# Performance work log

Hardware: AMD Instinct MI355X
Metric: run time of the kernel (lower is better)

The kernel has to match this reference:

```python
import jax, jax.numpy as jnp
import numpy as np

L, H, D, FF, T, S, N = 4, 16, 1024, 4096, 256, 256, 16
NEG = -1e9

def layer_norm(x, g, b):
    mu = jnp.mean(x, axis=-1, keepdims=True)
    var = jnp.var(x, axis=-1, keepdims=True)
    return (x - mu) / jnp.sqrt(var + 1e-5) * g + b

def mha(q_in, k_in, v_in, wq, bq, wk, bk, wv, bv, wo, bo, mask):
    # q_in: [T,N,D]; k_in/v_in: [S,N,D]
    t, n, d = q_in.shape
    s = k_in.shape[0]
    hd = d // H
    scale = hd ** -0.5
    q = (q_in @ wq.T + bq) * scale
    k = k_in @ wk.T + bk
    v = v_in @ wv.T + bv
    q = q.reshape(t, n, H, hd)
    k = k.reshape(s, n, H, hd)
    v = v.reshape(s, n, H, hd)
    scores = jnp.einsum('tnhd,snhd->nhts', q, k)  # [N,H,T,S]
    if mask is not None:
        scores = scores + mask  # mask [T,S] broadcasts
    a = jax.nn.softmax(scores, axis=-1)
    o = jnp.einsum('nhts,snhd->tnhd', a, v).reshape(t, n, d)
    return o @ wo.T + bo

def forward(tgt, memory, sa_wq, sa_bq, sa_wk, sa_bk, sa_wv, sa_bv, sa_wo, sa_bo,
            ca_wq, ca_bq, ca_wk, ca_bk, ca_wv, ca_bv, ca_wo, ca_bo,
            w1, b1, w2, b2, ln1_g, ln1_b, ln2_g, ln2_b, ln3_g, ln3_b, lnf_g, lnf_b):
    t = tgt.shape[0]
    causal = jnp.where(jnp.triu(jnp.ones((t, t), bool), 1), jnp.float32(NEG), jnp.float32(0.0))
    x = tgt
    for i in range(L):
        sa = mha(x, x, x, sa_wq[i], sa_bq[i], sa_wk[i], sa_bk[i], sa_wv[i], sa_bv[i], sa_wo[i], sa_bo[i], causal)
        x = layer_norm(x + sa, ln1_g[i], ln1_b[i])
        ca = mha(x, memory, memory, ca_wq[i], ca_bq[i], ca_wk[i], ca_bk[i], ca_wv[i], ca_bv[i], ca_wo[i], ca_bo[i], None)
        x = layer_norm(x + ca, ln2_g[i], ln2_b[i])
        ff = jax.nn.relu(x @ w1[i].T + b1[i]) @ w2[i].T + b2[i]
        x = layer_norm(x + ff, ln3_g[i], ln3_b[i])
    return layer_norm(x, lnf_g, lnf_b)

def setup_inputs() -> dict:
    key = jax.random.key(0)
    ks = iter(jax.random.split(key, 40))
    def nrm(shape, s):
        return (jax.random.normal(next(ks), shape, jnp.float32) * s).astype(jnp.float32)
    sd = D ** -0.5
    inp = {
        'tgt': nrm((T, N, D), 1.0),
        'memory': nrm((S, N, D), 1.0),
    }
    for pre in ('sa', 'ca'):
        for nm in ('wq', 'wk', 'wv', 'wo'):
            inp[f'{pre}_{nm}'] = nrm((L, D, D), sd)
        for nm in ('bq', 'bk', 'bv', 'bo'):
            inp[f'{pre}_{nm}'] = jnp.zeros((L, D), jnp.float32)
    inp['w1'] = nrm((L, FF, D), sd)
    inp['b1'] = jnp.zeros((L, FF), jnp.float32)
    inp['w2'] = nrm((L, D, FF), FF ** -0.5)
    inp['b2'] = jnp.zeros((L, D), jnp.float32)
    for nm in ('ln1', 'ln2', 'ln3'):
        inp[f'{nm}_g'] = jnp.ones((L, D), jnp.float32)
        inp[f'{nm}_b'] = jnp.zeros((L, D), jnp.float32)
    inp['lnf_g'] = jnp.ones((D,), jnp.float32)
    inp['lnf_b'] = jnp.zeros((D,), jnp.float32)
    return inp

def reference(tgt, memory, sa_wq, sa_bq, sa_wk, sa_bk, sa_wv, sa_bv, sa_wo, sa_bo,
              ca_wq, ca_bq, ca_wk, ca_bk, ca_wv, ca_bv, ca_wo, ca_bo,
              w1, b1, w2, b2, ln1_g, ln1_b, ln2_g, ln2_b, ln3_g, ln3_b, lnf_g, lnf_b):
    return forward(tgt, memory, sa_wq, sa_bq, sa_wk, sa_bk, sa_wv, sa_bv, sa_wo, sa_bo,
                   ca_wq, ca_bq, ca_wk, ca_bk, ca_wv, ca_bv, ca_wo, ca_bo,
                   w1, b1, w2, b2, ln1_g, ln1_b, ln2_g, ln2_b, ln3_g, ln3_b, lnf_g, lnf_b)
```

## Files before the change

kernel.cpp:

```cpp
#include <hip/hip_runtime.h>


typedef __attribute__((ext_vector_type(4))) float f32x4;
typedef __attribute__((ext_vector_type(8))) short bf16x8;
typedef __attribute__((ext_vector_type(4))) unsigned short u16x4;
typedef __attribute__((ext_vector_type(4))) unsigned int   u32x4;

__device__ __forceinline__ unsigned short f2bf(float f) {
    unsigned int u = __builtin_bit_cast(unsigned int, f);
    u += 0x7fffu + ((u >> 16) & 1u);
    return (unsigned short)(u >> 16);
}

__device__ __forceinline__ void gll16(const unsigned short* g, unsigned short* l) {
    auto* gp = reinterpret_cast<const __attribute__((address_space(1))) unsigned int*>(
        reinterpret_cast<uintptr_t>(g));
    auto* lp = reinterpret_cast<__attribute__((address_space(3))) unsigned int*>(
        reinterpret_cast<uintptr_t>(l));
    __builtin_amdgcn_global_load_lds(gp, lp, 16, 0, 0);
}

__device__ __forceinline__ void gemm_body(
    const unsigned short* __restrict__ A,
    const unsigned short* __restrict__ Bw,
    const float* __restrict__ bias,
    unsigned short* __restrict__ outb,
    float* __restrict__ po,
    int N, int lda, int klen, int mode,
    int m0, int n0, int kz,
    unsigned short (*Al)[128 * 32], unsigned short (*Bl)[128 * 32])
{
    const int tid  = threadIdx.x;
    const int lane = tid & 63;
    const int w    = tid >> 6;
    const int wr   = (w >> 1) * 64;
    const int wc   = (w & 1) * 64;
    const int l15  = lane & 15;
    const int l4   = lane >> 4;

    const int srow = w * 16 + (lane >> 2);
    const int scol = ((lane & 3) ^ ((srow >> 1) & 3)) * 8;
    const unsigned short* ag = A  + (size_t)(m0 + srow) * lda + kz + scol;
    const unsigned short* bg = Bw + (size_t)(n0 + srow) * lda + kz + scol;
    const size_t jstep = (size_t)64 * lda;
    const int lbase = (w * 16) * 32;

    int aoff[4], boff[4];
    #pragma unroll
    for (int i = 0; i < 4; ++i) {
        const int ra = wr + i * 16 + l15;
        const int rb = wc + i * 16 + l15;
        aoff[i] = ra * 32 + ((l4 ^ ((ra >> 1) & 3)) * 8);
        boff[i] = rb * 32 + ((l4 ^ ((rb >> 1) & 3)) * 8);
    }

    f32x4 acc[4][4];
    #pragma unroll
    for (int mi = 0; mi < 4; ++mi)
        #pragma unroll
        for (int ni = 0; ni < 4; ++ni)
            acc[mi][ni] = (f32x4){0.f, 0.f, 0.f, 0.f};

    #pragma unroll
    for (int j = 0; j < 2; ++j) {
        gll16(ag + j * jstep, &Al[0][lbase + j * 64 * 32]);
        gll16(bg + j * jstep, &Bl[0][lbase + j * 64 * 32]);
    }
    __syncthreads();

    const int nt = klen >> 5;
    int cur = 0;
    for (int t = 0; t < nt; ++t) {
        if (t + 1 < nt) {
            ag += 32; bg += 32;
            #pragma unroll
            for (int j = 0; j < 2; ++j) {
                gll16(ag + j * jstep, &Al[cur ^ 1][lbase + j * 64 * 32]);
                gll16(bg + j * jstep, &Bl[cur ^ 1][lbase + j * 64 * 32]);
            }
        }
        const unsigned short* ac = &Al[cur][0];
        const unsigned short* bc = &Bl[cur][0];
        bf16x8 af[4], bf[4];
        #pragma unroll
        for (int i = 0; i < 4; ++i) af[i] = *reinterpret_cast<const bf16x8*>(&ac[aoff[i]]);
        #pragma unroll
        for (int i = 0; i < 4; ++i) bf[i] = *reinterpret_cast<const bf16x8*>(&bc[boff[i]]);
        #pragma unroll
        for (int mi = 0; mi < 4; ++mi)
            #pragma unroll
            for (int ni = 0; ni < 4; ++ni)
                acc[mi][ni] = __builtin_amdgcn_mfma_f32_16x16x32_bf16(af[mi], bf[ni], acc[mi][ni], 0, 0, 0);
        __syncthreads();
        cur ^= 1;
    }

    #pragma unroll
    for (int mi = 0; mi < 4; ++mi) {
        #pragma unroll
        for (int ni = 0; ni < 4; ++ni) {
            const int col = n0 + wc + ni * 16 + l15;
            const float bs = (mode == 3) ? 0.f : bias[col];
            #pragma unroll
            for (int r = 0; r < 4; ++r) {
                const int row = m0 + wr + mi * 16 + l4 * 4 + r;
                const float val = acc[mi][ni][r] + bs;
                if (mode == 0)      outb[(size_t)row * N + col] = f2bf(val);
                else if (mode == 1) outb[(size_t)row * N + col] = f2bf(fmaxf(val, 0.f));
                else                po[(size_t)row * N + col] = val;
            }
        }
    }
}

__global__ __launch_bounds__(256, 4) void gemm128(
    const unsigned short* __restrict__ A,
    const unsigned short* __restrict__ Bw,
    const float* __restrict__ bias,
    unsigned short* __restrict__ outb,
    float* __restrict__ outf0,
    float* __restrict__ outf1,
    int N, int lda, int klen, int mode)
{
    __shared__ unsigned short Al[2][128 * 32];
    __shared__ unsigned short Bl[2][128 * 32];
    const int gx   = gridDim.x;
    const int orig = blockIdx.y * gx + blockIdx.x;
    const int xcd  = orig & 7;
    const int lin  = orig >> 3;
    const int m0   = (xcd * 4 + (lin & 3)) * 128;
    const int n0   = (lin >> 2) * 128;
    const int kz   = blockIdx.z * klen;
    float* po = (blockIdx.z == 0) ? outf0 : outf1;
    gemm_body(A, Bw, bias, outb, po, N, lda, klen, mode, m0, n0, kz, Al, Bl);
}

__global__ __launch_bounds__(256, 4) void gemm128_ca(
    const unsigned short* __restrict__ A0, const unsigned short* __restrict__ A1,
    const unsigned short* __restrict__ B0, const unsigned short* __restrict__ B1,
    const float* __restrict__ bias0, const float* __restrict__ bias1,
    unsigned short* __restrict__ out0, unsigned short* __restrict__ out1,
    int lda, int klen)
{
    __shared__ unsigned short Al[2][128 * 32];
    __shared__ unsigned short Bl[2][128 * 32];
    const int grp = (blockIdx.x >= 8);
    const int bx  = blockIdx.x - (grp ? 8 : 0);
    const int lgx = grp ? 16 : 8;
    const int orig = blockIdx.y * lgx + bx;
    const int xcd  = orig & 7;
    const int lin  = orig >> 3;
    const int m0   = (xcd * 4 + (lin & 3)) * 128;
    const int n0   = (lin >> 2) * 128;
    gemm_body(grp ? A1 : A0, grp ? B1 : B0, grp ? bias1 : bias0,
              grp ? out1 : out0, nullptr, grp ? 2048 : 1024, lda, klen, 0,
              m0, n0, 0, Al, Bl);
}

__global__ __launch_bounds__(128) void attn_fused(
    const unsigned short* __restrict__ Q, int qs,
    const unsigned short* __restrict__ Kb, int ks_,
    const unsigned short* __restrict__ Vb, int vs,
    unsigned short* __restrict__ O,
    int causal)
{
    __shared__ unsigned short Kl[8][256][8];
    __shared__ unsigned short Vt[32][64][8];
    __shared__ unsigned short Pl[2][32][16][8];
    const int tid   = threadIdx.x;
    const int lane  = tid & 63;
    const int w     = tid >> 6;
    const int bxi   = blockIdx.x;
    const int n     = bxi >> 5;
    const int h     = (bxi >> 1) & 15;
    const int thalf = bxi & 1;
    const int l15   = lane & 15;
    const int l4    = lane >> 4;
    const size_t hoff = (size_t)h * 64;

    #pragma unroll
    for (int i = 0; i < 16; ++i) {
        const int e = i * 128 + tid;
        const int s = e >> 3;
        const int c = e & 7;
        u32x4 kv = *reinterpret_cast<const u32x4*>(&Kb[((size_t)s * 16 + n) * ks_ + hoff + c * 8]);
        *reinterpret_cast<u32x4*>(&Kl[c][s][0]) = kv;
        u32x4 vv = *reinterpret_cast<const u32x4*>(&Vb[((size_t)s * 16 + n) * vs + hoff + c * 8]);
        const unsigned short* ve = reinterpret_cast<const unsigned short*>(&vv);
        #pragma unroll
        for (int j = 0; j < 8; ++j)
            Vt[s >> 3][c * 8 + j][s & 7] = ve[j];
    }
    __syncthreads();

    for (int ch = 0; ch < 4; ++ch) {
        const int t0 = thalf * 128 + w * 64 + ch * 16;
        bf16x8 qa[2];
        #pragma unroll
        for (int ks = 0; ks < 2; ++ks)
            qa[ks] = *reinterpret_cast<const bf16x8*>(
                &Q[((size_t)(t0 + l15) * 16 + n) * qs + hoff + ks * 32 + l4 * 8]);

        f32x4 sc[16];
        #pragma unroll
        for (int st = 0; st < 16; ++st) {
            if (causal && st * 16 > t0 + 15) {
                sc[st] = (f32x4){-1e9f, -1e9f, -1e9f, -1e9f};
                continue;
            }
            f32x4 a = (f32x4){0.f, 0.f, 0.f, 0.f};
            #pragma unroll
            for (int ks = 0; ks < 2; ++ks) {
                bf16x8 kf = *reinterpret_cast<const bf16x8*>(&Kl[ks * 4 + l4][st * 16 + l15][0]);
                a = __builtin_amdgcn_mfma_f32_16x16x32_bf16(qa[ks], kf, a, 0, 0, 0);
            }
            sc[st] = a;
        }
        if (causal) {
            #pragma unroll
            for (int st = 0; st < 16; ++st) {
                const int sg = st * 16 + l15;
                #pragma unroll
                for (int r = 0; r < 4; ++r) {
                    const int tg = t0 + l4 * 4 + r;
                    if (sg > tg) sc[st][r] = -1e9f;
                }
            }
        }
        #pragma unroll
        for (int r = 0; r < 4; ++r) {
            float mx = -3.0e38f;
            #pragma unroll
            for (int st = 0; st < 16; ++st) mx = fmaxf(mx, sc[st][r]);
            #pragma unroll
            for (int dd = 1; dd < 16; dd <<= 1) mx = fmaxf(mx, __shfl_xor(mx, dd, 64));
            float sum = 0.f;
            #pragma unroll
            for (int st = 0; st < 16; ++st) {
                const float e = __expf(sc[st][r] - mx);
                sc[st][r] = e;
                sum += e;
            }
            #pragma unroll
            for (int dd = 1; dd < 16; dd <<= 1) sum += __shfl_xor(sum, dd, 64);
            const float inv = 1.f / sum;
            const int rl = l4 * 4 + r;
            #pragma unroll
            for (int st = 0; st < 16; ++st) {
                const int sg = st * 16 + l15;
                Pl[w][sg >> 3][rl][sg & 7] = f2bf(sc[st][r] * inv);
            }
        }
        f32x4 oacc[4];
        #pragma unroll
        for (int dt = 0; dt < 4; ++dt) oacc[dt] = (f32x4){0.f, 0.f, 0.f, 0.f};
        #pragma unroll
        for (int kt = 0; kt < 8; ++kt) {
            if (causal && kt * 32 > t0 + 15) continue;
            bf16x8 pa = *reinterpret_cast<const bf16x8*>(&Pl[w][kt * 4 + l4][l15][0]);
            #pragma unroll
            for (int dt = 0; dt < 4; ++dt) {
                bf16x8 vf = *reinterpret_cast<const bf16x8*>(&Vt[kt * 4 + l4][dt * 16 + l15][0]);
                oacc[dt] = __builtin_amdgcn_mfma_f32_16x16x32_bf16(pa, vf, oacc[dt], 0, 0, 0);
            }
        }
        #pragma unroll
        for (int dt = 0; dt < 4; ++dt)
            #pragma unroll
            for (int r = 0; r < 4; ++r)
                O[((size_t)(t0 + l4 * 4 + r) * 16 + n) * 1024 + hoff + dt * 16 + l15] = f2bf(oacc[dt][r]);
    }
}

__device__ __forceinline__ void ln_body(
    f32x4 (&v)[4], int row, int lane,
    const float* __restrict__ g, const float* __restrict__ b,
    float* __restrict__ xf, unsigned short* __restrict__ xb)
{
    float s = 0.f;
    #pragma unroll
    for (int i = 0; i < 4; ++i) s += v[i][0] + v[i][1] + v[i][2] + v[i][3];
    #pragma unroll
    for (int dd = 1; dd < 64; dd <<= 1) s += __shfl_xor(s, dd, 64);
    const float mu = s * (1.f / 1024.f);
    float q = 0.f;
    #pragma unroll
    for (int i = 0; i < 4; ++i)
        #pragma unroll
        for (int j = 0; j < 4; ++j) { const float d0 = v[i][j] - mu; q += d0 * d0; }
    #pragma unroll
    for (int dd = 1; dd < 64; dd <<= 1) q += __shfl_xor(q, dd, 64);
    const float rstd = rsqrtf(q * (1.f / 1024.f) + 1e-5f);
    #pragma unroll
    for (int i = 0; i < 4; ++i) {
        const int col = i * 256 + lane * 4;
        f32x4 gg = *reinterpret_cast<const f32x4*>(&g[col]);
        f32x4 bb = *reinterpret_cast<const f32x4*>(&b[col]);
        f32x4 y;
        #pragma unroll
        for (int j = 0; j < 4; ++j) y[j] = (v[i][j] - mu) * rstd * gg[j] + bb[j];
        if (xf) *reinterpret_cast<f32x4*>(&xf[(size_t)row * 1024 + col]) = y;
        if (xb) {
            u16x4 pk;
            #pragma unroll
            for (int j = 0; j < 4; ++j) pk[j] = f2bf(y[j]);
            *reinterpret_cast<u16x4*>(&xb[(size_t)row * 1024 + col]) = pk;
        }
    }
}

__global__ __launch_bounds__(256) void ln_kernel(
    const float* __restrict__ z, const float* __restrict__ g, const float* __restrict__ b,
    float* __restrict__ xf, unsigned short* __restrict__ xb)
{
    const int row  = blockIdx.x * 4 + (threadIdx.x >> 6);
    const int lane = threadIdx.x & 63;
    f32x4 v[4];
    #pragma unroll
    for (int i = 0; i < 4; ++i)
        v[i] = *reinterpret_cast<const f32x4*>(&z[(size_t)row * 1024 + i * 256 + lane * 4]);
    ln_body(v, row, lane, g, b, xf, xb);
}

__global__ __launch_bounds__(256) void ln_red2(
    const float* __restrict__ p0, const float* __restrict__ p1,
    const float* __restrict__ bias, const float* __restrict__ resid,
    const float* __restrict__ g, const float* __restrict__ b,
    float* __restrict__ xf, unsigned short* __restrict__ xb)
{
    const int row  = blockIdx.x * 4 + (threadIdx.x >> 6);
    const int lane = threadIdx.x & 63;
    f32x4 v[4];
    #pragma unroll
    for (int i = 0; i < 4; ++i) {
        const int col = i * 256 + lane * 4;
        const size_t o = (size_t)row * 1024 + col;
        f32x4 a0 = *reinterpret_cast<const f32x4*>(&p0[o]);
        f32x4 a1 = *reinterpret_cast<const f32x4*>(&p1[o]);
        f32x4 bs = *reinterpret_cast<const f32x4*>(&bias[col]);
        f32x4 rs = *reinterpret_cast<const f32x4*>(&resid[o]);
        v[i] = a0 + a1 + bs + rs;
    }
    ln_body(v, row, lane, g, b, xf, xb);
}

__global__ __launch_bounds__(256) void cvt_bf16(
    const float* __restrict__ in, unsigned short* __restrict__ out, int n)
{
    const int i = (blockIdx.x * 256 + threadIdx.x) * 4;
    if (i >= n) return;
    f32x4 v = *reinterpret_cast<const f32x4*>(&in[i]);
    u16x4 pk;
    #pragma unroll
    for (int j = 0; j < 4; ++j) pk[j] = f2bf(v[j]);
    *reinterpret_cast<u16x4*>(&out[i]) = pk;
}

__global__ __launch_bounds__(256) void pack_layer_w(
    const float* __restrict__ sa_wq, const float* __restrict__ sa_wk, const float* __restrict__ sa_wv,
    const float* __restrict__ ca_wq, const float* __restrict__ ca_wk, const float* __restrict__ ca_wv,
    const float* __restrict__ sa_wo, const float* __restrict__ ca_wo,
    const float* __restrict__ w1,   const float* __restrict__ w2,
    unsigned short* __restrict__ dst, int layer)
{
    const size_t DD = 1024u * 1024u;
    const size_t e  = ((size_t)blockIdx.x * 256 + threadIdx.x) * 4;
    const float* src;
    float scale = 1.f;
    if (e < 3 * DD) {
        const int part = (int)(e / DD);
        src = (part == 0 ? sa_wq : part == 1 ? sa_wk : sa_wv) + layer * DD + (e % DD);
        if (part == 0) scale = 0.125f;
    } else if (e < 6 * DD) {
        const size_t r = e - 3 * DD;
        const int part = (int)(r / DD);
        src = (part == 0 ? ca_wq : part == 1 ? ca_wk : ca_wv) + layer * DD + (r % DD);
        if (part == 0) scale = 0.125f;
    } else if (e < 7 * DD)  { src = sa_wo + layer * DD + (e - 6 * DD); }
    else if (e < 8 * DD)    { src = ca_wo + layer * DD + (e - 7 * DD); }
    else if (e < 12 * DD)   { src = w1 + (size_t)layer * 4 * DD + (e - 8 * DD); }
    else                    { src = w2 + (size_t)layer * 4 * DD + (e - 12 * DD); }
    f32x4 v = *reinterpret_cast<const f32x4*>(src);
    u16x4 pk;
    #pragma unroll
    for (int j = 0; j < 4; ++j) pk[j] = f2bf(v[j] * scale);
    *reinterpret_cast<u16x4*>(&dst[e]) = pk;
}

__global__ __launch_bounds__(256) void pack_bias(
    const float* __restrict__ sa_bq, const float* __restrict__ sa_bk, const float* __restrict__ sa_bv,
    const float* __restrict__ ca_bq, const float* __restrict__ ca_bk, const float* __restrict__ ca_bv,
    float* __restrict__ sab, float* __restrict__ cab)
{
    const int idx = blockIdx.x * 256 + threadIdx.x;
    const int half = idx / 12288;
    const int r    = idx % 12288;
    const int l    = r / 3072;
    const int pc   = r % 3072;
    const int part = pc >> 10;
    const int c    = pc & 1023;
    const float* src = half == 0 ? (part == 0 ? sa_bq : part == 1 ? sa_bk : sa_bv)
                                 : (part == 0 ? ca_bq : part == 1 ? ca_bk : ca_bv);
    const float v = src[l * 1024 + c] * (part == 0 ? 0.125f : 1.f);
    (half ? cab : sab)[l * 3072 + pc] = v;
}

extern "C" void kernel_launch(void* const* d_in, const int* in_sizes, int n_in,
                              void* d_out, int out_size, void* d_ws, size_t ws_size,
                              hipStream_t stream)
{
    (void)in_sizes; (void)n_in; (void)out_size; (void)ws_size;
    const int M  = 4096;
    const int Dm = 1024;
    const size_t DD = (size_t)Dm * Dm;

    const float* tgt   = (const float*)d_in[0];
    const float* mem   = (const float*)d_in[1];
    const float* sa_wq = (const float*)d_in[2];
    const float* sa_wk = (const float*)d_in[3];
    const float* sa_wv = (const float*)d_in[4];
    const float* sa_wo = (const float*)d_in[5];
    const float* sa_bq = (const float*)d_in[6];
    const float* sa_bk = (const float*)d_in[7];
    const float* sa_bv = (const float*)d_in[8];
    const float* sa_bo = (const float*)d_in[9];
    const float* ca_wq = (const float*)d_in[10];
    const float* ca_wk = (const float*)d_in[11];
    const float* ca_wv = (const float*)d_in[12];
    const float* ca_wo = (const float*)d_in[13];
    const float* ca_bq = (const float*)d_in[14];
    const float* ca_bk = (const float*)d_in[15];
    const float* ca_bv = (const float*)d_in[16];
    const float* ca_bo = (const float*)d_in[17];
    const float* w1    = (const float*)d_in[18];
    const float* b1    = (const float*)d_in[19];
    const float* w2    = (const float*)d_in[20];
    const float* b2    = (const float*)d_in[21];
    const float* ln1g  = (const float*)d_in[22];
    const float* ln1b  = (const float*)d_in[23];
    const float* ln2g  = (const float*)d_in[24];
    const float* ln2b  = (const float*)d_in[25];
    const float* ln3g  = (const float*)d_in[26];
    const float* ln3b  = (const float*)d_in[27];
    const float* lnfg  = (const float*)d_in[28];
    const float* lnfb  = (const float*)d_in[29];

    char* p = (char*)d_ws;
    float*          x_f    = (float*)p;          p += (size_t)M * Dm * 4;
    unsigned short* x_b    = (unsigned short*)p; p += (size_t)M * Dm * 2;
    unsigned short* mem_b  = (unsigned short*)p; p += (size_t)M * Dm * 2;
    unsigned short* qkv_b  = (unsigned short*)p; p += (size_t)M * 3072 * 2;
    unsigned short* cakv_b = (unsigned short*)p; p += (size_t)M * 2048 * 2;
    unsigned short* caq_b  = (unsigned short*)p; p += (size_t)M * Dm * 2;
    unsigned short* ao_b   = (unsigned short*)p; p += (size_t)M * Dm * 2;
    unsigned short* wpack  = (unsigned short*)p; p += 16 * DD * 2;
    float*          sab    = (float*)p;          p += 4 * 3072 * 4;
    float*          cab    = (float*)p;          p += 4 * 3072 * 4;
    unsigned short* h_b    = qkv_b;
    float*          parA   = (float*)qkv_b;
    float*          parB   = (float*)cakv_b;
    float*          par0   = (float*)((char*)qkv_b + (size_t)M * 4096 * 2);
    float*          par1   = (float*)wpack;

    dim3 blk(256), blkA(128);

    cvt_bf16<<<4096, blk, 0, stream>>>(tgt, x_b, M * Dm);
    cvt_bf16<<<4096, blk, 0, stream>>>(mem, mem_b, M * Dm);
    pack_bias<<<96, blk, 0, stream>>>(sa_bq, sa_bk, sa_bv, ca_bq, ca_bk, ca_bv, sab, cab);

    const float* res = tgt;
    for (int i = 0; i < 4; ++i) {
        pack_layer_w<<<16384, blk, 0, stream>>>(sa_wq, sa_wk, sa_wv, ca_wq, ca_wk, ca_wv,
                                                sa_wo, ca_wo, w1, w2, wpack, i);
        gemm128<<<dim3(24, 32, 1), blk, 0, stream>>>(x_b, wpack, sab + i * 3072,
            qkv_b, nullptr, nullptr, 3072, 1024, 1024, 0);
        attn_fused<<<512, blkA, 0, stream>>>(qkv_b, 3072, qkv_b + 1024, 3072, qkv_b + 2048, 3072, ao_b, 1);
        gemm128<<<dim3(8, 32, 2), blk, 0, stream>>>(ao_b, wpack + 6 * DD, nullptr,
            nullptr, parA, parB, 1024, 1024, 512, 3);
        ln_red2<<<1024, blk, 0, stream>>>(parA, parB, sa_bo + i * Dm, res,
            ln1g + i * Dm, ln1b + i * Dm, x_f, x_b);
        res = x_f;
        gemm128_ca<<<dim3(24, 32, 1), blk, 0, stream>>>(x_b, mem_b,
            wpack + 3 * DD, wpack + 4 * DD,
            cab + i * 3072, cab + i * 3072 + 1024,
            caq_b, cakv_b, 1024, 1024);
        attn_fused<<<512, blkA, 0, stream>>>(caq_b, 1024, cakv_b, 2048, cakv_b + 1024, 2048, ao_b, 0);
        gemm128<<<dim3(8, 32, 2), blk, 0, stream>>>(ao_b, wpack + 7 * DD, nullptr,
            nullptr, parA, parB, 1024, 1024, 512, 3);
        ln_red2<<<1024, blk, 0, stream>>>(parA, parB, ca_bo + i * Dm, x_f,
            ln2g + i * Dm, ln2b + i * Dm, x_f, x_b);
        gemm128<<<dim3(32, 32, 1), blk, 0, stream>>>(x_b, wpack + 8 * DD, b1 + i * 4096,
            h_b, nullptr, nullptr, 4096, 1024, 1024, 1);
        gemm128<<<dim3(8, 32, 2), blk, 0, stream>>>(h_b, wpack + 12 * DD, nullptr,
            nullptr, par0, par1, 1024, 4096, 2048, 3);
        ln_red2<<<1024, blk, 0, stream>>>(par0, par1, b2 + i * Dm, x_f,
            ln3g + i * Dm, ln3b + i * Dm, x_f, x_b);
    }
    ln_kernel<<<1024, blk, 0, stream>>>(x_f, lnfg, lnfb, (float*)d_out, nullptr);
}
```

Before: 1.323 ms.

## Triple-buffer GEMM LDS tiles with prefetch distance two and explicit vmcnt waits

```diff
diff --git a/kernel.cpp b/kernel.cpp
--- a/kernel.cpp
+++ b/kernel.cpp
@@ -19,6 +19,8 @@
         reinterpret_cast<uintptr_t>(l));
     __builtin_amdgcn_global_load_lds(gp, lp, 16, 0, 0);
 }
+
+#define SB0() __builtin_amdgcn_sched_barrier(0)
 
 __device__ __forceinline__ void gemm_body(
     const unsigned short* __restrict__ A,
@@ -61,26 +63,33 @@
         for (int ni = 0; ni < 4; ++ni)
             acc[mi][ni] = (f32x4){0.f, 0.f, 0.f, 0.f};
 
-    #pragma unroll
-    for (int j = 0; j < 2; ++j) {
-        gll16(ag + j * jstep, &Al[0][lbase + j * 64 * 32]);
-        gll16(bg + j * jstep, &Bl[0][lbase + j * 64 * 32]);
-    }
-    __syncthreads();
+    auto stage = [&](int buf, int tt) {
+        const unsigned short* a = ag + tt * 32;
+        const unsigned short* b = bg + tt * 32;
+        gll16(a,         &Al[buf][lbase]);
+        gll16(a + jstep, &Al[buf][lbase + 64 * 32]);
+        gll16(b,         &Bl[buf][lbase]);
+        gll16(b + jstep, &Bl[buf][lbase + 64 * 32]);
+    };
 
     const int nt = klen >> 5;
-    int cur = 0;
+    stage(0, 0);
+    if (nt > 1) stage(1, 1);
+
+    int rd = 0, st = 2;
     for (int t = 0; t < nt; ++t) {
-        if (t + 1 < nt) {
-            ag += 32; bg += 32;
-            #pragma unroll
-            for (int j = 0; j < 2; ++j) {
-                gll16(ag + j * jstep, &Al[cur ^ 1][lbase + j * 64 * 32]);
-                gll16(bg + j * jstep, &Bl[cur ^ 1][lbase + j * 64 * 32]);
-            }
-        }
-        const unsigned short* ac = &Al[cur][0];
-        const unsigned short* bc = &Bl[cur][0];
+        if (t + 2 < nt) stage(st, t + 2);
+        const int rem = nt - 1 - t;
+        SB0();
+        if (rem >= 2)      asm volatile("s_waitcnt vmcnt(8)" ::: "memory");
+        else if (rem == 1) asm volatile("s_waitcnt vmcnt(4)" ::: "memory");
+        else               asm volatile("s_waitcnt vmcnt(0)" ::: "memory");
+        SB0();
+        __builtin_amdgcn_s_barrier();
+        SB0();
+
+        const unsigned short* ac = &Al[rd][0];
+        const unsigned short* bc = &Bl[rd][0];
         bf16x8 af[4], bf[4];
         #pragma unroll
         for (int i = 0; i < 4; ++i) af[i] = *reinterpret_cast<const bf16x8*>(&ac[aoff[i]]);
@@ -91,8 +100,10 @@
             #pragma unroll
             for (int ni = 0; ni < 4; ++ni)
                 acc[mi][ni] = __builtin_amdgcn_mfma_f32_16x16x32_bf16(af[mi], bf[ni], acc[mi][ni], 0, 0, 0);
-        __syncthreads();
-        cur ^= 1;
+        SB0();
+        __builtin_amdgcn_s_barrier();
+        rd = (rd == 2) ? 0 : rd + 1;
+        st = (st == 2) ? 0 : st + 1;
     }
 
     #pragma unroll
@@ -113,7 +124,7 @@
     }
 }
 
-__global__ __launch_bounds__(256, 4) void gemm128(
+__global__ __launch_bounds__(256, 3) void gemm128(
     const unsigned short* __restrict__ A,
     const unsigned short* __restrict__ Bw,
     const float* __restrict__ bias,
@@ -122,8 +133,8 @@
     float* __restrict__ outf1,
     int N, int lda, int klen, int mode)
 {
-    __shared__ unsigned short Al[2][128 * 32];
-    __shared__ unsigned short Bl[2][128 * 32];
+    __shared__ unsigned short Al[3][128 * 32];
+    __shared__ unsigned short Bl[3][128 * 32];
     const int gx   = gridDim.x;
     const int orig = blockIdx.y * gx + blockIdx.x;
     const int xcd  = orig & 7;
@@ -135,15 +146,15 @@
     gemm_body(A, Bw, bias, outb, po, N, lda, klen, mode, m0, n0, kz, Al, Bl);
 }
 
-__global__ __launch_bounds__(256, 4) void gemm128_ca(
+__global__ __launch_bounds__(256, 3) void gemm128_ca(
     const unsigned short* __restrict__ A0, const unsigned short* __restrict__ A1,
     const unsigned short* __restrict__ B0, const unsigned short* __restrict__ B1,
     const float* __restrict__ bias0, const float* __restrict__ bias1,
     unsigned short* __restrict__ out0, unsigned short* __restrict__ out1,
     int lda, int klen)
 {
-    __shared__ unsigned short Al[2][128 * 32];
-    __shared__ unsigned short Bl[2][128 * 32];
+    __shared__ unsigned short Al[3][128 * 32];
+    __shared__ unsigned short Bl[3][128 * 32];
     const int grp = (blockIdx.x >= 8);
     const int bx  = blockIdx.x - (grp ? 8 : 0);
     const int lgx = grp ? 16 : 8;
```

New measurement: 1.334 ms. About the same (+0.8%).

## Load GEMM A-operand fragments directly from global into registers, bypassing LDS

Applied to the files above, without the earlier changes.

```diff
diff --git a/kernel.cpp b/kernel.cpp
--- a/kernel.cpp
+++ b/kernel.cpp
@@ -28,7 +28,7 @@
     float* __restrict__ po,
     int N, int lda, int klen, int mode,
     int m0, int n0, int kz,
-    unsigned short (*Al)[128 * 32], unsigned short (*Bl)[128 * 32])
+    unsigned short (*Bl)[128 * 32])
 {
     const int tid  = threadIdx.x;
     const int lane = tid & 63;
@@ -40,19 +40,19 @@
 
     const int srow = w * 16 + (lane >> 2);
     const int scol = ((lane & 3) ^ ((srow >> 1) & 3)) * 8;
-    const unsigned short* ag = A  + (size_t)(m0 + srow) * lda + kz + scol;
     const unsigned short* bg = Bw + (size_t)(n0 + srow) * lda + kz + scol;
     const size_t jstep = (size_t)64 * lda;
     const int lbase = (w * 16) * 32;
 
-    int aoff[4], boff[4];
+    int boff[4];
     #pragma unroll
     for (int i = 0; i < 4; ++i) {
-        const int ra = wr + i * 16 + l15;
         const int rb = wc + i * 16 + l15;
-        aoff[i] = ra * 32 + ((l4 ^ ((ra >> 1) & 3)) * 8);
         boff[i] = rb * 32 + ((l4 ^ ((rb >> 1) & 3)) * 8);
     }
+
+    const unsigned short* ab = A + (size_t)(m0 + wr + l15) * lda + kz + l4 * 8;
+    const size_t astep = (size_t)16 * lda;
 
     f32x4 acc[4][4];
     #pragma unroll
@@ -61,38 +61,57 @@
         for (int ni = 0; ni < 4; ++ni)
             acc[mi][ni] = (f32x4){0.f, 0.f, 0.f, 0.f};
 
-    #pragma unroll
-    for (int j = 0; j < 2; ++j) {
-        gll16(ag + j * jstep, &Al[0][lbase + j * 64 * 32]);
+    bf16x8 afA[4], afB[4];
+    #pragma unroll
+    for (int i = 0; i < 4; ++i)
+        afA[i] = *reinterpret_cast<const bf16x8*>(ab + (size_t)i * astep);
+    #pragma unroll
+    for (int j = 0; j < 2; ++j)
         gll16(bg + j * jstep, &Bl[0][lbase + j * 64 * 32]);
-    }
     __syncthreads();
 
     const int nt = klen >> 5;
-    int cur = 0;
-    for (int t = 0; t < nt; ++t) {
+    for (int t = 0; t < nt; t += 2) {
         if (t + 1 < nt) {
-            ag += 32; bg += 32;
-            #pragma unroll
-            for (int j = 0; j < 2; ++j) {
-                gll16(ag + j * jstep, &Al[cur ^ 1][lbase + j * 64 * 32]);
-                gll16(bg + j * jstep, &Bl[cur ^ 1][lbase + j * 64 * 32]);
-            }
-        }
-        const unsigned short* ac = &Al[cur][0];
-        const unsigned short* bc = &Bl[cur][0];
-        bf16x8 af[4], bf[4];
-        #pragma unroll
-        for (int i = 0; i < 4; ++i) af[i] = *reinterpret_cast<const bf16x8*>(&ac[aoff[i]]);
-        #pragma unroll
-        for (int i = 0; i < 4; ++i) bf[i] = *reinterpret_cast<const bf16x8*>(&bc[boff[i]]);
-        #pragma unroll
-        for (int mi = 0; mi < 4; ++mi)
-            #pragma unroll
-            for (int ni = 0; ni < 4; ++ni)
-                acc[mi][ni] = __builtin_amdgcn_mfma_f32_16x16x32_bf16(af[mi], bf[ni], acc[mi][ni], 0, 0, 0);
+            #pragma unroll
+            for (int j = 0; j < 2; ++j)
+                gll16(bg + (t + 1) * 32 + j * jstep, &Bl[1][lbase + j * 64 * 32]);
+            #pragma unroll
+            for (int i = 0; i < 4; ++i)
+                afB[i] = *reinterpret_cast<const bf16x8*>(ab + (t + 1) * 32 + (size_t)i * astep);
+        }
+        {
+            const unsigned short* bc = &Bl[0][0];
+            bf16x8 bf[4];
+            #pragma unroll
+            for (int i = 0; i < 4; ++i) bf[i] = *reinterpret_cast<const bf16x8*>(&bc[boff[i]]);
+            #pragma unroll
+            for (int mi = 0; mi < 4; ++mi)
+                #pragma unroll
+                for (int ni = 0; ni < 4; ++ni)
+                    acc[mi][ni] = __builtin_amdgcn_mfma_f32_16x16x32_bf16(afA[mi], bf[ni], acc[mi][ni], 0, 0, 0);
+        }
         __syncthreads();
-        cur ^= 1;
+        if (t + 1 < nt) {
+            if (t + 2 < nt) {
+                #pragma unroll
+                for (int j = 0; j < 2; ++j)
+                    gll16(bg + (t + 2) * 32 + j * jstep, &Bl[0][lbase + j * 64 * 32]);
+                #pragma unroll
+                for (int i = 0; i < 4; ++i)
+                    afA[i] = *reinterpret_cast<const bf16x8*>(ab + (t + 2) * 32 + (size_t)i * astep);
+            }
+            const unsigned short* bc = &Bl[1][0];
+            bf16x8 bf[4];
+            #pragma unroll
+            for (int i = 0; i < 4; ++i) bf[i] = *reinterpret_cast<const bf16x8*>(&bc[boff[i]]);
+            #pragma unroll
+            for (int mi = 0; mi < 4; ++mi)
+                #pragma unroll
+                for (int ni = 0; ni < 4; ++ni)
+                    acc[mi][ni] = __builtin_amdgcn_mfma_f32_16x16x32_bf16(afB[mi], bf[ni], acc[mi][ni], 0, 0, 0);
+            __syncthreads();
+        }
     }
 
     #pragma unroll
@@ -122,7 +141,6 @@
     float* __restrict__ outf1,
     int N, int lda, int klen, int mode)
 {
-    __shared__ unsigned short Al[2][128 * 32];
     __shared__ unsigned short Bl[2][128 * 32];
     const int gx   = gridDim.x;
     const int orig = blockIdx.y * gx + blockIdx.x;
@@ -132,7 +150,7 @@
     const int n0   = (lin >> 2) * 128;
     const int kz   = blockIdx.z * klen;
     float* po = (blockIdx.z == 0) ? outf0 : outf1;
-    gemm_body(A, Bw, bias, outb, po, N, lda, klen, mode, m0, n0, kz, Al, Bl);
+    gemm_body(A, Bw, bias, outb, po, N, lda, klen, mode, m0, n0, kz, Bl);
 }
 
 __global__ __launch_bounds__(256, 4) void gemm128_ca(
@@ -142,7 +160,6 @@
     unsigned short* __restrict__ out0, unsigned short* __restrict__ out1,
     int lda, int klen)
 {
-    __shared__ unsigned short Al[2][128 * 32];
     __shared__ unsigned short Bl[2][128 * 32];
     const int grp = (blockIdx.x >= 8);
     const int bx  = blockIdx.x - (grp ? 8 : 0);
@@ -154,7 +171,7 @@
     const int n0   = (lin >> 2) * 128;
     gemm_body(grp ? A1 : A0, grp ? B1 : B0, grp ? bias1 : bias0,
               grp ? out1 : out0, nullptr, grp ? 2048 : 1024, lda, klen, 0,
-              m0, n0, 0, Al, Bl);
+              m0, n0, 0, Bl);
 }
 
 __global__ __launch_bounds__(128) void attn_fused(
```

Result: slower. 2.079 ms (+57.1%).

## Store split-K partial sums in bf16 and merge input conversion launches

Applied to the files above, without the earlier changes.

```diff
diff --git a/kernel.cpp b/kernel.cpp
--- a/kernel.cpp
+++ b/kernel.cpp
@@ -10,6 +10,9 @@
     unsigned int u = __builtin_bit_cast(unsigned int, f);
     u += 0x7fffu + ((u >> 16) & 1u);
     return (unsigned short)(u >> 16);
+}
+__device__ __forceinline__ float bf2f(unsigned short u) {
+    return __builtin_bit_cast(float, (unsigned int)u << 16);
 }
 
 __device__ __forceinline__ void gll16(const unsigned short* g, unsigned short* l) {
@@ -25,7 +28,7 @@
     const unsigned short* __restrict__ Bw,
     const float* __restrict__ bias,
     unsigned short* __restrict__ outb,
-    float* __restrict__ po,
+    unsigned short* __restrict__ po,
     int N, int lda, int klen, int mode,
     int m0, int n0, int kz,
     unsigned short (*Al)[128 * 32], unsigned short (*Bl)[128 * 32])
@@ -107,7 +110,7 @@
                 const float val = acc[mi][ni][r] + bs;
                 if (mode == 0)      outb[(size_t)row * N + col] = f2bf(val);
                 else if (mode == 1) outb[(size_t)row * N + col] = f2bf(fmaxf(val, 0.f));
-                else                po[(size_t)row * N + col] = val;
+                else                po[(size_t)row * N + col] = f2bf(val);
             }
         }
     }
@@ -118,8 +121,8 @@
     const unsigned short* __restrict__ Bw,
     const float* __restrict__ bias,
     unsigned short* __restrict__ outb,
-    float* __restrict__ outf0,
-    float* __restrict__ outf1,
+    unsigned short* __restrict__ pb0,
+    unsigned short* __restrict__ pb1,
     int N, int lda, int klen, int mode)
 {
     __shared__ unsigned short Al[2][128 * 32];
@@ -131,7 +134,7 @@
     const int m0   = (xcd * 4 + (lin & 3)) * 128;
     const int n0   = (lin >> 2) * 128;
     const int kz   = blockIdx.z * klen;
-    float* po = (blockIdx.z == 0) ? outf0 : outf1;
+    unsigned short* po = (blockIdx.z == 0) ? pb0 : pb1;
     gemm_body(A, Bw, bias, outb, po, N, lda, klen, mode, m0, n0, kz, Al, Bl);
 }
 
@@ -323,7 +326,7 @@
 }
 
 __global__ __launch_bounds__(256) void ln_red2(
-    const float* __restrict__ p0, const float* __restrict__ p1,
+    const unsigned short* __restrict__ p0, const unsigned short* __restrict__ p1,
     const float* __restrict__ bias, const float* __restrict__ resid,
     const float* __restrict__ g, const float* __restrict__ b,
     float* __restrict__ xf, unsigned short* __restrict__ xb)
@@ -335,25 +338,30 @@
     for (int i = 0; i < 4; ++i) {
         const int col = i * 256 + lane * 4;
         const size_t o = (size_t)row * 1024 + col;
-        f32x4 a0 = *reinterpret_cast<const f32x4*>(&p0[o]);
-        f32x4 a1 = *reinterpret_cast<const f32x4*>(&p1[o]);
+        u16x4 a0 = *reinterpret_cast<const u16x4*>(&p0[o]);
+        u16x4 a1 = *reinterpret_cast<const u16x4*>(&p1[o]);
         f32x4 bs = *reinterpret_cast<const f32x4*>(&bias[col]);
         f32x4 rs = *reinterpret_cast<const f32x4*>(&resid[o]);
-        v[i] = a0 + a1 + bs + rs;
+        #pragma unroll
+        for (int j = 0; j < 4; ++j)
+            v[i][j] = bf2f(a0[j]) + bf2f(a1[j]) + bs[j] + rs[j];
     }
     ln_body(v, row, lane, g, b, xf, xb);
 }
 
-__global__ __launch_bounds__(256) void cvt_bf16(
-    const float* __restrict__ in, unsigned short* __restrict__ out, int n)
+__global__ __launch_bounds__(256) void cvt2_bf16(
+    const float* __restrict__ in0, const float* __restrict__ in1,
+    unsigned short* __restrict__ out0, unsigned short* __restrict__ out1, int n0)
 {
     const int i = (blockIdx.x * 256 + threadIdx.x) * 4;
-    if (i >= n) return;
-    f32x4 v = *reinterpret_cast<const f32x4*>(&in[i]);
+    const float* src = (i < n0) ? in0 : in1;
+    unsigned short* dst = (i < n0) ? out0 : out1;
+    const int off = (i < n0) ? i : i - n0;
+    f32x4 v = *reinterpret_cast<const f32x4*>(&src[off]);
     u16x4 pk;
     #pragma unroll
     for (int j = 0; j < 4; ++j) pk[j] = f2bf(v[j]);
-    *reinterpret_cast<u16x4*>(&out[i]) = pk;
+    *reinterpret_cast<u16x4*>(&dst[off]) = pk;
 }
 
 __global__ __launch_bounds__(256) void pack_layer_w(
@@ -457,15 +465,14 @@
     float*          sab    = (float*)p;          p += 4 * 3072 * 4;
     float*          cab    = (float*)p;          p += 4 * 3072 * 4;
     unsigned short* h_b    = qkv_b;
-    float*          parA   = (float*)qkv_b;
-    float*          parB   = (float*)cakv_b;
-    float*          par0   = (float*)((char*)qkv_b + (size_t)M * 4096 * 2);
-    float*          par1   = (float*)wpack;
+    unsigned short* parA   = qkv_b;
+    unsigned short* parB   = cakv_b;
+    unsigned short* par0   = (unsigned short*)((char*)qkv_b + (size_t)M * 4096 * 2);
+    unsigned short* par1   = wpack;
 
     dim3 blk(256), blkA(128);
 
-    cvt_bf16<<<4096, blk, 0, stream>>>(tgt, x_b, M * Dm);
-    cvt_bf16<<<4096, blk, 0, stream>>>(mem, mem_b, M * Dm);
+    cvt2_bf16<<<8192, blk, 0, stream>>>(tgt, mem, x_b, mem_b, M * Dm);
     pack_bias<<<96, blk, 0, stream>>>(sa_bq, sa_bk, sa_bv, ca_bq, ca_bk, ca_bv, sab, cab);
 
     const float* res = tgt;
```

After: 1.275 ms. -3.6%, faster.
